# Kernel optimization log

Hardware: AMD Instinct MI355X
Metric: run time of the kernel (lower is better)

Reference implementation:

```python
import jax, jax.numpy as jnp
import numpy as np

N = 50000      # nodes
E = 400000     # edges per relation
R = 3          # edge types
D = 128        # input_dim == hidden_dim
H = 8          # attention heads
Dh = D // H    # per-head dim (16)
OUT = 1        # output logits
NEG_SLOPE = 0.2
LN_EPS = 1e-5


def setup_inputs() -> dict:
    key = jax.random.key(0)
    ks = jax.random.split(key, 20)
    s = 0.05
    f32 = jnp.float32
    return {
        "feat": jax.random.normal(ks[0], (N, D), f32),
        "edge_src": jax.random.randint(ks[1], (R, E), 0, N, dtype=jnp.int32),
        "edge_dst": jax.random.randint(ks[2], (R, E), 0, N, dtype=jnp.int32),
        # conv1: per-relation GATConv params (W, attn_l, attn_r, bias)
        "W1": jax.random.normal(ks[3], (R, D, H * Dh), f32) * s,
        "al1": jax.random.normal(ks[4], (R, H, Dh), f32) * s,
        "ar1": jax.random.normal(ks[5], (R, H, Dh), f32) * s,
        "b1": jnp.zeros((R, H * Dh), f32),
        # conv2
        "W2": jax.random.normal(ks[6], (R, D, H * Dh), f32) * s,
        "al2": jax.random.normal(ks[7], (R, H, Dh), f32) * s,
        "ar2": jax.random.normal(ks[8], (R, H, Dh), f32) * s,
        "b2": jnp.zeros((R, H * Dh), f32),
        # LayerNorm
        "ln_g": jnp.ones((D,), f32),
        "ln_b": jnp.zeros((D,), f32),
        # classifier MLP (dropout inactive at eval)
        "Wc1": jax.random.normal(ks[9], (D, D), f32) * s,
        "bc1": jnp.zeros((D,), f32),
        "Wc2": jax.random.normal(ks[10], (D, OUT), f32) * s,
        "bc2": jnp.zeros((OUT,), f32),
    }


def _gat(x, src, dst, W, al, ar, b):
    """DGL GATConv on one relation: x [N,Din] -> [N, H*Dh]."""
    h = (x @ W).reshape(N, H, Dh)                       # projected feats
    el = (h * al).sum(-1)                               # [N,H] src attn term
    er = (h * ar).sum(-1)                               # [N,H] dst attn term
    e = jax.nn.leaky_relu(el[src] + er[dst], NEG_SLOPE)  # [E,H]
    # edge-softmax over incoming edges per dst node, per head
    m = jax.ops.segment_max(e, dst, num_segments=N)     # [N,H]
    ex = jnp.exp(e - m[dst])
    denom = jax.ops.segment_sum(ex, dst, num_segments=N)
    alpha = ex / denom[dst]                             # [E,H]
    msg = alpha[:, :, None] * h[src]                    # [E,H,Dh]
    out = jax.ops.segment_sum(msg, dst, num_segments=N)  # [N,H,Dh]
    return out.reshape(N, H * Dh) + b


def _hetero(x, edge_src, edge_dst, W, al, ar, b):
    out = jnp.zeros((N, H * Dh), x.dtype)
    for r in range(R):  # small fixed relation count
        out = out + _gat(x, edge_src[r], edge_dst[r], W[r], al[r], ar[r], b[r])
    return out


def reference(feat, edge_src, edge_dst, W1, al1, ar1, b1, W2, al2, ar2, b2,
              ln_g, ln_b, Wc1, bc1, Wc2, bc2):
    h1 = jax.nn.relu(_hetero(feat, edge_src, edge_dst, W1, al1, ar1, b1))
    h2 = _hetero(h1, edge_src, edge_dst, W2, al2, ar2, b2)
    h = h2 + h1
    mu = h.mean(-1, keepdims=True)
    var = ((h - mu) ** 2).mean(-1, keepdims=True)
    h = (h - mu) * jax.lax.rsqrt(var + LN_EPS) * ln_g + ln_b
    h = jax.nn.relu(h @ Wc1 + bc1)
    return h @ Wc2 + bc2
```

## Files before the change

### kernel.cpp

```cpp
#include <hip/hip_runtime.h>
#include <math.h>

#define NN 50000
#define NE 400000
#define NREL 3
#define NCH 196

typedef __bf16 bf16x8 __attribute__((ext_vector_type(8)));
typedef float floatx4 __attribute__((ext_vector_type(4)));

__device__ __forceinline__ unsigned short f2bf(float f) {
  unsigned int u = __float_as_uint(f);
  return (unsigned short)((u + 0x7fffu + ((u >> 16) & 1u)) >> 16);
}

__global__ __launch_bounds__(256) void prep_wt(
    const float* __restrict__ W1, const float* __restrict__ W2,
    const float* __restrict__ Wc1, unsigned short* __restrict__ Wt) {
  int mat = blockIdx.x >> 3, slab = blockIdx.x & 7;
  const float* Wsrc = mat < 3 ? W1 + mat * 16384
                    : (mat < 6 ? W2 + (mat - 3) * 16384 : Wc1);
  unsigned short* dst = Wt + (size_t)mat * 144 * 128;
  int k0 = slab * 16;
#pragma unroll
  for (int i = 0; i < 8; ++i) {
    int idx = i * 256 + threadIdx.x;
    int k = k0 + (idx >> 7), nn = idx & 127;
    dst[nn * 128 + k] = f2bf(Wsrc[k * 128 + nn]);
  }
}

__global__ __launch_bounds__(256) void prep_attn(
    const float* __restrict__ W1, const float* __restrict__ W2,
    const float* __restrict__ al1, const float* __restrict__ ar1,
    const float* __restrict__ al2, const float* __restrict__ ar2,
    unsigned short* __restrict__ Wt) {
  int mat = blockIdx.x;
  const float* Wsrc = mat < 3 ? W1 + mat * 16384 : W2 + (mat - 3) * 16384;
  const float* alp = mat < 3 ? al1 + mat * 128 : al2 + (mat - 3) * 128;
  const float* arp = mat < 3 ? ar1 + mat * 128 : ar2 + (mat - 3) * 128;
  unsigned short* dst = Wt + (size_t)mat * 144 * 128;
#pragma unroll
  for (int i = 0; i < 8; ++i) {
    int j = i * 256 + threadIdx.x;
    int half = j >> 10, jj = j & 1023;
    int k = jj >> 3, h = jj & 7;
    const float* av = half ? arp : alp;
    float s = 0.f;
#pragma unroll
    for (int d = 0; d < 16; ++d) s += Wsrc[k * 128 + h * 16 + d] * av[h * 16 + d];
    dst[(128 + half * 8 + h) * 128 + k] = f2bf(s);
  }
}

__global__ __launch_bounds__(256) void gemm3_attn_mfma(
    const float* __restrict__ X, const unsigned short* __restrict__ Wt,
    unsigned short* __restrict__ hp, float* __restrict__ el,
    float* __restrict__ er, int n) {
  __shared__ unsigned short Xs[64 * 136];
  __shared__ unsigned short Ws[144 * 136];
  int t = threadIdx.x;
  int rowbase = blockIdx.x * 64;

  const float4* X4 = (const float4*)X;
#pragma unroll
  for (int i = 0; i < 8; ++i) {
    int v = t + i * 256;
    int row = v >> 5, k4 = (v & 31) * 4;
    float4 x = make_float4(0.f, 0.f, 0.f, 0.f);
    if (rowbase + row < n) x = X4[(size_t)(rowbase + row) * 32 + (v & 31)];
    ushort4 p;
    p.x = f2bf(x.x); p.y = f2bf(x.y); p.z = f2bf(x.z); p.w = f2bf(x.w);
    *(ushort4*)&Xs[row * 136 + k4] = p;
  }

  int lane = t & 63, wave = t >> 6;
  int quad = lane >> 4, l = lane & 15;

  for (int r = 0; r < NREL; ++r) {
    __syncthreads();
    const uint4* WtR = (const uint4*)(Wt + (size_t)r * 144 * 128);
#pragma unroll
    for (int i = 0; i < 9; ++i) {
      int v = t + i * 256;
      ((uint4*)Ws)[(v >> 4) * 17 + (v & 15)] = WtR[v];
    }
    __syncthreads();

    floatx4 acc[9];
#pragma unroll
    for (int i = 0; i < 9; ++i) acc[i] = floatx4{0.f, 0.f, 0.f, 0.f};
#pragma unroll
    for (int ks = 0; ks < 4; ++ks) {
      bf16x8 a = *(const bf16x8*)&Xs[(wave * 16 + l) * 136 + ks * 32 + quad * 8];
#pragma unroll
      for (int nt = 0; nt < 9; ++nt) {
        bf16x8 b = *(const bf16x8*)&Ws[(nt * 16 + l) * 136 + ks * 32 + quad * 8];
        acc[nt] = __builtin_amdgcn_mfma_f32_16x16x32_bf16(a, b, acc[nt], 0, 0, 0);
      }
    }

    unsigned short* hpR = hp + (size_t)r * NN * 128;
    float* elR = el + (size_t)r * NN * 8;
    float* erR = er + (size_t)r * NN * 8;
    int r0 = rowbase + wave * 16 + quad * 4;
#pragma unroll
    for (int reg = 0; reg < 4; ++reg) {
      int row = r0 + reg;
      if (row < n) {
#pragma unroll
        for (int nt = 0; nt < 8; ++nt)
          hpR[(size_t)row * 128 + nt * 16 + l] = f2bf(acc[nt][reg]);
        if (l < 8) elR[row * 8 + l] = acc[8][reg];
        else       erR[row * 8 + (l - 8)] = acc[8][reg];
      }
    }
  }
}

__global__ __launch_bounds__(256) void gemm_head_mfma(
    const float* __restrict__ X, const unsigned short* __restrict__ Wt,
    const float* __restrict__ bc1, const float* __restrict__ wc2,
    const float* __restrict__ bc2, float* __restrict__ out, int n) {
  __shared__ unsigned short Xs[64 * 136];
  __shared__ unsigned short Ws[128 * 136];
  int t = threadIdx.x;
  int rowbase = blockIdx.x * 64;

  const float4* X4 = (const float4*)X;
#pragma unroll
  for (int i = 0; i < 8; ++i) {
    int v = t + i * 256;
    int row = v >> 5, k4 = (v & 31) * 4;
    float4 x = make_float4(0.f, 0.f, 0.f, 0.f);
    if (rowbase + row < n) x = X4[(size_t)(rowbase + row) * 32 + (v & 31)];
    ushort4 p;
    p.x = f2bf(x.x); p.y = f2bf(x.y); p.z = f2bf(x.z); p.w = f2bf(x.w);
    *(ushort4*)&Xs[row * 136 + k4] = p;
  }
  const uint4* WtR = (const uint4*)Wt;
#pragma unroll
  for (int i = 0; i < 8; ++i) {
    int v = t + i * 256;
    ((uint4*)Ws)[(v >> 4) * 17 + (v & 15)] = WtR[v];
  }
  __syncthreads();

  int lane = t & 63, wave = t >> 6;
  int quad = lane >> 4, l = lane & 15;

  floatx4 acc[8];
#pragma unroll
  for (int i = 0; i < 8; ++i) acc[i] = floatx4{0.f, 0.f, 0.f, 0.f};
#pragma unroll
  for (int ks = 0; ks < 4; ++ks) {
    bf16x8 a = *(const bf16x8*)&Xs[(wave * 16 + l) * 136 + ks * 32 + quad * 8];
#pragma unroll
    for (int nt = 0; nt < 8; ++nt) {
      bf16x8 b = *(const bf16x8*)&Ws[(nt * 16 + l) * 136 + ks * 32 + quad * 8];
      acc[nt] = __builtin_amdgcn_mfma_f32_16x16x32_bf16(a, b, acc[nt], 0, 0, 0);
    }
  }

  float bv[8], wv[8];
#pragma unroll
  for (int nt = 0; nt < 8; ++nt) {
    bv[nt] = bc1[nt * 16 + l];
    wv[nt] = wc2[nt * 16 + l];
  }
  int r0 = rowbase + wave * 16 + quad * 4;
#pragma unroll
  for (int reg = 0; reg < 4; ++reg) {
    float s = 0.f;
#pragma unroll
    for (int nt = 0; nt < 8; ++nt)
      s += fmaxf(acc[nt][reg] + bv[nt], 0.f) * wv[nt];
    s += __shfl_xor(s, 1); s += __shfl_xor(s, 2);
    s += __shfl_xor(s, 4); s += __shfl_xor(s, 8);
    int row = r0 + reg;
    if (l == 0 && row < n) out[row] = s + bc2[0];
  }
}

__global__ __launch_bounds__(256) void hist_kernel(
    const int* __restrict__ edst, int* __restrict__ cnt, int* __restrict__ rank) {
  int t = blockIdx.x * 256 + threadIdx.x;
  if (t >= NREL * NE) return;
  int r = t / NE;
  rank[t] = atomicAdd(&cnt[r * NN + edst[t]], 1);
}

__global__ __launch_bounds__(256) void scan1(
    const int* __restrict__ cnt, int* __restrict__ partials) {
  __shared__ int s[256];
  int r = blockIdx.x / NCH, c = blockIdx.x % NCH;
  int i = c * 256 + threadIdx.x;
  s[threadIdx.x] = (i < NN) ? cnt[r * NN + i] : 0;
  __syncthreads();
  for (int off = 128; off; off >>= 1) {
    if (threadIdx.x < off) s[threadIdx.x] += s[threadIdx.x + off];
    __syncthreads();
  }
  if (threadIdx.x == 0) partials[r * NCH + c] = s[0];
}

__global__ __launch_bounds__(256) void scan2(int* __restrict__ partials) {
  __shared__ int s[256];
  int r = blockIdx.x;
  int t = threadIdx.x;
  int v = (t < NCH) ? partials[r * NCH + t] : 0;
  s[t] = v;
  __syncthreads();
  for (int off = 1; off < 256; off <<= 1) {
    int x = (t >= off) ? s[t - off] : 0;
    __syncthreads();
    s[t] += x;
    __syncthreads();
  }
  if (t < NCH) partials[r * NCH + t] = s[t] - v;
}

__global__ __launch_bounds__(256) void scan3(
    const int* __restrict__ cnt, const int* __restrict__ partials,
    int* __restrict__ rowptr) {
  __shared__ int s[256];
  int r = blockIdx.x / NCH, c = blockIdx.x % NCH;
  int t = threadIdx.x;
  int i = c * 256 + t;
  int v = (i < NN) ? cnt[r * NN + i] : 0;
  s[t] = v;
  __syncthreads();
  for (int off = 1; off < 256; off <<= 1) {
    int x = (t >= off) ? s[t - off] : 0;
    __syncthreads();
    s[t] += x;
    __syncthreads();
  }
  int base = partials[r * NCH + c];
  if (i < NN) rowptr[r * (NN + 1) + i] = base + s[t] - v;
  if (c == NCH - 1 && t == 0) rowptr[r * (NN + 1) + NN] = NE;
}

__global__ __launch_bounds__(256) void scatter_kernel(
    const int* __restrict__ esrc, const int* __restrict__ edst,
    const int* __restrict__ rowptr, const int* __restrict__ rank,
    int* __restrict__ col) {
  int t = blockIdx.x * 256 + threadIdx.x;
  if (t >= NREL * NE) return;
  int r = t / NE;
  int pos = rowptr[r * (NN + 1) + edst[t]] + rank[t];
  col[(size_t)r * NE + pos] = esrc[t];
}

__global__ __launch_bounds__(256) void gather_all(
    const int* __restrict__ rowptr, const int* __restrict__ col,
    const float* __restrict__ el, const float* __restrict__ er,
    const unsigned short* __restrict__ hp, const float* __restrict__ b,
    float* __restrict__ h1, const float* __restrict__ g,
    const float* __restrict__ beta, int mode) {
  int wid = (blockIdx.x * 256 + threadIdx.x) >> 6;
  int lane = threadIdx.x & 63;
  if (wid >= NN) return;
  int h = lane >> 3;
  int eoff = lane & 7;
  int c = lane * 2;
  int lane4 = lane * 4;

  int st0, st1, st2, ee0, ee1, ee2;
  {
    const int* rp = rowptr;
    st0 = rp[wid]; ee0 = rp[wid + 1];
    rp += NN + 1;
    st1 = rp[wid]; ee1 = rp[wid + 1];
    rp += NN + 1;
    st2 = rp[wid]; ee2 = rp[wid + 1];
  }
  float erv0 = er[wid * 8 + h];
  float erv1 = er[(size_t)NN * 8 + wid * 8 + h];
  float erv2 = er[(size_t)2 * NN * 8 + wid * 8 + h];
  float b0x = b[c], b1x = b[128 + c], b2x = b[256 + c];
  float b0y = b[c + 1], b1y = b[128 + c + 1], b2y = b[256 + c + 1];
  float2* hptr = (float2*)&h1[(size_t)wid * 128 + c];
  float2 r1 = make_float2(0.f, 0.f);
  float gx = 0.f, gy = 0.f, btx = 0.f, bty = 0.f;
  if (mode) {
    r1 = *hptr;
    gx = g[c]; gy = g[c + 1];
    btx = beta[c]; bty = beta[c + 1];
  }

  const int* clp0 = col;
  const int* clp1 = col + NE;
  const int* clp2 = col + 2 * NE;
  const float* elp0 = el;
  const float* elp1 = el + (size_t)NN * 8;
  const float* elp2 = el + (size_t)2 * NN * 8;
  const char* hpb0 = (const char*)hp;
  const char* hpb1 = hpb0 + (size_t)NN * 256;
  const char* hpb2 = hpb1 + (size_t)NN * 256;

  int la0 = ee0 - 1; if (la0 < st0) la0 = st0; if (la0 >= NE) la0 = NE - 1;
  int la1 = ee1 - 1; if (la1 < st1) la1 = st1; if (la1 >= NE) la1 = NE - 1;
  int la2 = ee2 - 1; if (la2 < st2) la2 = st2; if (la2 >= NE) la2 = NE - 1;

  int i0 = st0 + eoff, i1 = st1 + eoff, i2 = st2 + eoff;
  int cv0 = clp0[i0 < la0 ? i0 : la0];
  int cv1 = clp1[i1 < la1 ? i1 : la1];
  int cv2 = clp2[i2 < la2 ? i2 : la2];
  float ev0 = elp0[cv0 * 8 + h];
  float ev1 = elp1[cv1 * 8 + h];
  float ev2 = elp2[cv2 * 8 + h];

  int bb0 = st0, bb1 = st1, bb2 = st2;
  float den0 = 0.f, den1 = 0.f, den2 = 0.f;
  float sx0 = 0.f, sy0 = 0.f, sx1 = 0.f, sy1 = 0.f, sx2 = 0.f, sy2 = 0.f;

#define A_PHASE(R)                                                             \
  if (a##R) {                                                                  \
    int ni_ = bb##R + 8 + eoff;                                                \
    cm##R = clp##R[ni_ < la##R ? ni_ : la##R];                                 \
    float e_ = ev##R + erv##R;                                                 \
    e_ = fmaxf(e_, 0.2f * e_);                                                 \
    float x_ = (bb##R + eoff < ee##R) ? __expf(e_) : 0.f;                      \
    den##R += x_;                                                              \
    xi##R = __float_as_uint(x_);                                               \
  }

#define LOAD_EDGE(R, JJ)                                                       \
  {                                                                            \
    int s_ = __builtin_amdgcn_readlane(cv##R, JJ);                             \
    u##R##_##JJ = *(const unsigned int*)(hpb##R + (size_t)s_ * 256 + lane4);   \
  }

#define B_PHASE(R)                                                             \
  if (a##R) {                                                                  \
    LOAD_EDGE(R, 0) LOAD_EDGE(R, 1) LOAD_EDGE(R, 2) LOAD_EDGE(R, 3)            \
    LOAD_EDGE(R, 4) LOAD_EDGE(R, 5) LOAD_EDGE(R, 6) LOAD_EDGE(R, 7)            \
  }

#define FMA_EDGE(R, JJ, PAT)                                                   \
  {                                                                            \
    float xe_ = __uint_as_float(__builtin_amdgcn_ds_swizzle(xi##R, PAT));      \
    sx##R += xe_ * __uint_as_float(u##R##_##JJ << 16);                         \
    sy##R += xe_ * __uint_as_float(u##R##_##JJ & 0xffff0000u);                 \
  }

#define C_PHASE(R)                                                             \
  if (a##R) {                                                                  \
    FMA_EDGE(R, 0, 0x18) FMA_EDGE(R, 1, 0x38) FMA_EDGE(R, 2, 0x58)             \
    FMA_EDGE(R, 3, 0x78) FMA_EDGE(R, 4, 0x98) FMA_EDGE(R, 5, 0xb8)             \
    FMA_EDGE(R, 6, 0xd8) FMA_EDGE(R, 7, 0xf8)                                  \
  }

  for (;;) {
    bool a0 = bb0 < ee0, a1 = bb1 < ee1, a2 = bb2 < ee2;
    if (!(a0 | a1 | a2)) break;
    int cm0 = cv0, cm1 = cv1, cm2 = cv2;
    unsigned int xi0 = 0, xi1 = 0, xi2 = 0;
    unsigned int u0_0, u0_1, u0_2, u0_3, u0_4, u0_5, u0_6, u0_7;
    unsigned int u1_0, u1_1, u1_2, u1_3, u1_4, u1_5, u1_6, u1_7;
    unsigned int u2_0, u2_1, u2_2, u2_3, u2_4, u2_5, u2_6, u2_7;
    A_PHASE(0) A_PHASE(1) A_PHASE(2)
    B_PHASE(0) B_PHASE(1) B_PHASE(2)
    float evn0 = ev0, evn1 = ev1, evn2 = ev2;
    if (a0) evn0 = elp0[cm0 * 8 + h];
    if (a1) evn1 = elp1[cm1 * 8 + h];
    if (a2) evn2 = elp2[cm2 * 8 + h];
    __builtin_amdgcn_sched_barrier(0);
    C_PHASE(0) C_PHASE(1) C_PHASE(2)
    bb0 += 8; bb1 += 8; bb2 += 8;
    cv0 = cm0; cv1 = cm1; cv2 = cm2;
    ev0 = evn0; ev1 = evn1; ev2 = evn2;
  }

#undef A_PHASE
#undef LOAD_EDGE
#undef B_PHASE
#undef FMA_EDGE
#undef C_PHASE

  float ax = 0.f, ay = 0.f;
  if (ee0 > st0) {
    float d = den0;
    d += __shfl_xor(d, 1); d += __shfl_xor(d, 2); d += __shfl_xor(d, 4);
    float inv = 1.f / d;
    ax += sx0 * inv; ay += sy0 * inv;
  }
  if (ee1 > st1) {
    float d = den1;
    d += __shfl_xor(d, 1); d += __shfl_xor(d, 2); d += __shfl_xor(d, 4);
    float inv = 1.f / d;
    ax += sx1 * inv; ay += sy1 * inv;
  }
  if (ee2 > st2) {
    float d = den2;
    d += __shfl_xor(d, 1); d += __shfl_xor(d, 2); d += __shfl_xor(d, 4);
    float inv = 1.f / d;
    ax += sx2 * inv; ay += sy2 * inv;
  }

  float bx = b0x + b1x + b2x;
  float by = b0y + b1y + b2y;
  if (mode == 0) {
    *hptr = make_float2(fmaxf(ax + bx, 0.f), fmaxf(ay + by, 0.f));
  } else {
    float vx = ax + bx + r1.x;
    float vy = ay + by + r1.y;
    float s = vx + vy;
#pragma unroll
    for (int off = 32; off; off >>= 1) s += __shfl_xor(s, off);
    float mu = s * (1.f / 128.f);
    float dx = vx - mu, dy = vy - mu;
    float sq = dx * dx + dy * dy;
#pragma unroll
    for (int off = 32; off; off >>= 1) sq += __shfl_xor(sq, off);
    float rstd = rsqrtf(sq * (1.f / 128.f) + 1e-5f);
    *hptr = make_float2(dx * rstd * gx + btx, dy * rstd * gy + bty);
  }
}

extern "C" void kernel_launch(void* const* d_in, const int* in_sizes, int n_in,
                              void* d_out, int out_size, void* d_ws, size_t ws_size,
                              hipStream_t stream) {
  const float* feat = (const float*)d_in[0];
  const int* esrc = (const int*)d_in[1];
  const int* edst = (const int*)d_in[2];
  const float* W1 = (const float*)d_in[3];
  const float* al1 = (const float*)d_in[4];
  const float* ar1 = (const float*)d_in[5];
  const float* b1 = (const float*)d_in[6];
  const float* W2 = (const float*)d_in[7];
  const float* al2 = (const float*)d_in[8];
  const float* ar2 = (const float*)d_in[9];
  const float* b2 = (const float*)d_in[10];
  const float* lng = (const float*)d_in[11];
  const float* lnb = (const float*)d_in[12];
  const float* Wc1 = (const float*)d_in[13];
  const float* bc1 = (const float*)d_in[14];
  const float* Wc2 = (const float*)d_in[15];
  const float* bc2 = (const float*)d_in[16];
  float* out = (float*)d_out;

  unsigned short* hp = (unsigned short*)d_ws;
  float* el = (float*)(hp + (size_t)3 * NN * 128);
  float* er = el + (size_t)3 * NN * 8;
  float* h1 = er + (size_t)3 * NN * 8;
  int* rowptr = (int*)(h1 + (size_t)NN * 128);
  int* col = rowptr + NREL * (NN + 1);
  int* cnt = col + (size_t)NREL * NE;
  int* partials = cnt + NREL * NN;
  unsigned short* Wt = (unsigned short*)(((uintptr_t)(partials + NREL * NCH) + 15)
                                         & ~(uintptr_t)15);
  int* rank = (int*)el;

  const int gemm_grid = (NN + 63) / 64;
  const int edge_grid = (NREL * NE + 255) / 256;
  const int gg_grid = (NN * 64) / 256;

  prep_wt<<<56, 256, 0, stream>>>(W1, W2, Wc1, Wt);
  prep_attn<<<6, 256, 0, stream>>>(W1, W2, al1, ar1, al2, ar2, Wt);

  (void)hipMemsetAsync(cnt, 0, (size_t)NREL * NN * sizeof(int), stream);
  hist_kernel<<<edge_grid, 256, 0, stream>>>(edst, cnt, rank);
  scan1<<<NREL * NCH, 256, 0, stream>>>(cnt, partials);
  scan2<<<NREL, 256, 0, stream>>>(partials);
  scan3<<<NREL * NCH, 256, 0, stream>>>(cnt, partials, rowptr);
  scatter_kernel<<<edge_grid, 256, 0, stream>>>(esrc, edst, rowptr, rank, col);

  gemm3_attn_mfma<<<gemm_grid, 256, 0, stream>>>(feat, Wt, hp, el, er, NN);
  gather_all<<<gg_grid, 256, 0, stream>>>(rowptr, col, el, er, hp, b1,
                                          h1, nullptr, nullptr, 0);
  gemm3_attn_mfma<<<gemm_grid, 256, 0, stream>>>(
      h1, Wt + (size_t)3 * 144 * 128, hp, el, er, NN);
  gather_all<<<gg_grid, 256, 0, stream>>>(rowptr, col, el, er, hp, b2,
                                          h1, lng, lnb, 1);
  gemm_head_mfma<<<gemm_grid, 256, 0, stream>>>(
      h1, Wt + (size_t)6 * 144 * 128, bc1, Wc2, bc2, out, NN);
}
```

Baseline: 420.2 us.

## Peel first 8-edge chunk of all relations unconditionally, per-relation tail loops

Restructures the gather kernel so the first block of up to 8 edges for all three relations is loaded and accumulated without branching, with all 24 feature loads issued together. The remaining edges are processed in separate per-relation loops. Bias, residual and LayerNorm parameter loads move to the epilogue to free registers during the main gather. The aim is more memory-level parallelism and fewer loop-control branches for the typical low-degree node, at the cost of serialising the relations in the tail and issuing loads for relations that have no edges.

```diff
diff --git a/kernel.cpp b/kernel.cpp
--- a/kernel.cpp
+++ b/kernel.cpp
@@ -266,28 +266,15 @@
   int c = lane * 2;
   int lane4 = lane * 4;
 
-  int st0, st1, st2, ee0, ee1, ee2;
-  {
-    const int* rp = rowptr;
-    st0 = rp[wid]; ee0 = rp[wid + 1];
-    rp += NN + 1;
-    st1 = rp[wid]; ee1 = rp[wid + 1];
-    rp += NN + 1;
-    st2 = rp[wid]; ee2 = rp[wid + 1];
-  }
+  const int* rp0 = rowptr;
+  const int* rp1 = rowptr + (NN + 1);
+  const int* rp2 = rowptr + 2 * (NN + 1);
+  int st0 = rp0[wid], ee0 = rp0[wid + 1];
+  int st1 = rp1[wid], ee1 = rp1[wid + 1];
+  int st2 = rp2[wid], ee2 = rp2[wid + 1];
   float erv0 = er[wid * 8 + h];
   float erv1 = er[(size_t)NN * 8 + wid * 8 + h];
   float erv2 = er[(size_t)2 * NN * 8 + wid * 8 + h];
-  float b0x = b[c], b1x = b[128 + c], b2x = b[256 + c];
-  float b0y = b[c + 1], b1y = b[128 + c + 1], b2y = b[256 + c + 1];
-  float2* hptr = (float2*)&h1[(size_t)wid * 128 + c];
-  float2 r1 = make_float2(0.f, 0.f);
-  float gx = 0.f, gy = 0.f, btx = 0.f, bty = 0.f;
-  if (mode) {
-    r1 = *hptr;
-    gx = g[c]; gy = g[c + 1];
-    btx = beta[c]; bty = beta[c + 1];
-  }
 
   const int* clp0 = col;
   const int* clp1 = col + NE;
@@ -304,80 +291,132 @@
   int la2 = ee2 - 1; if (la2 < st2) la2 = st2; if (la2 >= NE) la2 = NE - 1;
 
   int i0 = st0 + eoff, i1 = st1 + eoff, i2 = st2 + eoff;
+  int j0 = i0 + 8, j1 = i1 + 8, j2 = i2 + 8;
   int cv0 = clp0[i0 < la0 ? i0 : la0];
   int cv1 = clp1[i1 < la1 ? i1 : la1];
   int cv2 = clp2[i2 < la2 ? i2 : la2];
+  int cm0 = clp0[j0 < la0 ? j0 : la0];
+  int cm1 = clp1[j1 < la1 ? j1 : la1];
+  int cm2 = clp2[j2 < la2 ? j2 : la2];
+
   float ev0 = elp0[cv0 * 8 + h];
   float ev1 = elp1[cv1 * 8 + h];
   float ev2 = elp2[cv2 * 8 + h];
 
-  int bb0 = st0, bb1 = st1, bb2 = st2;
-  float den0 = 0.f, den1 = 0.f, den2 = 0.f;
-  float sx0 = 0.f, sy0 = 0.f, sx1 = 0.f, sy1 = 0.f, sx2 = 0.f, sy2 = 0.f;
-
-#define A_PHASE(R)                                                             \
-  if (a##R) {                                                                  \
-    int ni_ = bb##R + 8 + eoff;                                                \
-    cm##R = clp##R[ni_ < la##R ? ni_ : la##R];                                 \
-    float e_ = ev##R + erv##R;                                                 \
-    e_ = fmaxf(e_, 0.2f * e_);                                                 \
-    float x_ = (bb##R + eoff < ee##R) ? __expf(e_) : 0.f;                      \
-    den##R += x_;                                                              \
-    xi##R = __float_as_uint(x_);                                               \
-  }
-
-#define LOAD_EDGE(R, JJ)                                                       \
+  unsigned int u0_0, u0_1, u0_2, u0_3, u0_4, u0_5, u0_6, u0_7;
+  unsigned int u1_0, u1_1, u1_2, u1_3, u1_4, u1_5, u1_6, u1_7;
+  unsigned int u2_0, u2_1, u2_2, u2_3, u2_4, u2_5, u2_6, u2_7;
+
+#define LOAD1(R, JJ)                                                           \
   {                                                                            \
     int s_ = __builtin_amdgcn_readlane(cv##R, JJ);                             \
     u##R##_##JJ = *(const unsigned int*)(hpb##R + (size_t)s_ * 256 + lane4);   \
   }
-
-#define B_PHASE(R)                                                             \
-  if (a##R) {                                                                  \
-    LOAD_EDGE(R, 0) LOAD_EDGE(R, 1) LOAD_EDGE(R, 2) LOAD_EDGE(R, 3)            \
-    LOAD_EDGE(R, 4) LOAD_EDGE(R, 5) LOAD_EDGE(R, 6) LOAD_EDGE(R, 7)            \
-  }
-
-#define FMA_EDGE(R, JJ, PAT)                                                   \
+  LOAD1(0, 0) LOAD1(0, 1) LOAD1(0, 2) LOAD1(0, 3)
+  LOAD1(0, 4) LOAD1(0, 5) LOAD1(0, 6) LOAD1(0, 7)
+  LOAD1(1, 0) LOAD1(1, 1) LOAD1(1, 2) LOAD1(1, 3)
+  LOAD1(1, 4) LOAD1(1, 5) LOAD1(1, 6) LOAD1(1, 7)
+  LOAD1(2, 0) LOAD1(2, 1) LOAD1(2, 2) LOAD1(2, 3)
+  LOAD1(2, 4) LOAD1(2, 5) LOAD1(2, 6) LOAD1(2, 7)
+#undef LOAD1
+
+  float e0 = ev0 + erv0; e0 = fmaxf(e0, 0.2f * e0);
+  float e1 = ev1 + erv1; e1 = fmaxf(e1, 0.2f * e1);
+  float e2 = ev2 + erv2; e2 = fmaxf(e2, 0.2f * e2);
+  float x0 = (i0 < ee0) ? __expf(e0) : 0.f;
+  float x1 = (i1 < ee1) ? __expf(e1) : 0.f;
+  float x2 = (i2 < ee2) ? __expf(e2) : 0.f;
+  float den0 = x0, den1 = x1, den2 = x2;
+  unsigned int xi0 = __float_as_uint(x0);
+  unsigned int xi1 = __float_as_uint(x1);
+  unsigned int xi2 = __float_as_uint(x2);
+
+  float sx0 = 0.f, sy0 = 0.f, sx1 = 0.f, sy1 = 0.f, sx2 = 0.f, sy2 = 0.f;
+
+#define FMA1(R, JJ, PAT)                                                       \
   {                                                                            \
     float xe_ = __uint_as_float(__builtin_amdgcn_ds_swizzle(xi##R, PAT));      \
     sx##R += xe_ * __uint_as_float(u##R##_##JJ << 16);                         \
     sy##R += xe_ * __uint_as_float(u##R##_##JJ & 0xffff0000u);                 \
   }
-
-#define C_PHASE(R)                                                             \
-  if (a##R) {                                                                  \
-    FMA_EDGE(R, 0, 0x18) FMA_EDGE(R, 1, 0x38) FMA_EDGE(R, 2, 0x58)             \
-    FMA_EDGE(R, 3, 0x78) FMA_EDGE(R, 4, 0x98) FMA_EDGE(R, 5, 0xb8)             \
-    FMA_EDGE(R, 6, 0xd8) FMA_EDGE(R, 7, 0xf8)                                  \
-  }
-
-  for (;;) {
-    bool a0 = bb0 < ee0, a1 = bb1 < ee1, a2 = bb2 < ee2;
-    if (!(a0 | a1 | a2)) break;
-    int cm0 = cv0, cm1 = cv1, cm2 = cv2;
-    unsigned int xi0 = 0, xi1 = 0, xi2 = 0;
-    unsigned int u0_0, u0_1, u0_2, u0_3, u0_4, u0_5, u0_6, u0_7;
-    unsigned int u1_0, u1_1, u1_2, u1_3, u1_4, u1_5, u1_6, u1_7;
-    unsigned int u2_0, u2_1, u2_2, u2_3, u2_4, u2_5, u2_6, u2_7;
-    A_PHASE(0) A_PHASE(1) A_PHASE(2)
-    B_PHASE(0) B_PHASE(1) B_PHASE(2)
-    float evn0 = ev0, evn1 = ev1, evn2 = ev2;
-    if (a0) evn0 = elp0[cm0 * 8 + h];
-    if (a1) evn1 = elp1[cm1 * 8 + h];
-    if (a2) evn2 = elp2[cm2 * 8 + h];
-    __builtin_amdgcn_sched_barrier(0);
-    C_PHASE(0) C_PHASE(1) C_PHASE(2)
-    bb0 += 8; bb1 += 8; bb2 += 8;
-    cv0 = cm0; cv1 = cm1; cv2 = cm2;
-    ev0 = evn0; ev1 = evn1; ev2 = evn2;
-  }
-
-#undef A_PHASE
-#undef LOAD_EDGE
-#undef B_PHASE
-#undef FMA_EDGE
-#undef C_PHASE
+  FMA1(0, 0, 0x18) FMA1(0, 1, 0x38) FMA1(0, 2, 0x58) FMA1(0, 3, 0x78)
+  FMA1(0, 4, 0x98) FMA1(0, 5, 0xb8) FMA1(0, 6, 0xd8) FMA1(0, 7, 0xf8)
+  FMA1(1, 0, 0x18) FMA1(1, 1, 0x38) FMA1(1, 2, 0x58) FMA1(1, 3, 0x78)
+  FMA1(1, 4, 0x98) FMA1(1, 5, 0xb8) FMA1(1, 6, 0xd8) FMA1(1, 7, 0xf8)
+  FMA1(2, 0, 0x18) FMA1(2, 1, 0x38) FMA1(2, 2, 0x58) FMA1(2, 3, 0x78)
+  FMA1(2, 4, 0x98) FMA1(2, 5, 0xb8) FMA1(2, 6, 0xd8) FMA1(2, 7, 0xf8)
+#undef FMA1
+
+#define TAIL(R)                                                                \
+  if (st##R + 8 < ee##R) {                                                     \
+    int bb = st##R + 8;                                                        \
+    int cvt = cm##R;                                                           \
+    float evt = elp##R[cvt * 8 + h];                                           \
+    for (;;) {                                                                 \
+      int ni = bb + 8 + eoff;                                                  \
+      int cmt = clp##R[ni < la##R ? ni : la##R];                               \
+      float e_ = evt + erv##R;                                                 \
+      e_ = fmaxf(e_, 0.2f * e_);                                               \
+      float x_ = (bb + eoff < ee##R) ? __expf(e_) : 0.f;                       \
+      den##R += x_;                                                            \
+      unsigned int xt_ = __float_as_uint(x_);                                  \
+      unsigned int t0, t1, t2, t3, t4, t5, t6, t7;                             \
+      {                                                                        \
+        int s_;                                                                \
+        s_ = __builtin_amdgcn_readlane(cvt, 0);                                \
+        t0 = *(const unsigned int*)(hpb##R + (size_t)s_ * 256 + lane4);        \
+        s_ = __builtin_amdgcn_readlane(cvt, 1);                                \
+        t1 = *(const unsigned int*)(hpb##R + (size_t)s_ * 256 + lane4);        \
+        s_ = __builtin_amdgcn_readlane(cvt, 2);                                \
+        t2 = *(const unsigned int*)(hpb##R + (size_t)s_ * 256 + lane4);        \
+        s_ = __builtin_amdgcn_readlane(cvt, 3);                                \
+        t3 = *(const unsigned int*)(hpb##R + (size_t)s_ * 256 + lane4);        \
+        s_ = __builtin_amdgcn_readlane(cvt, 4);                                \
+        t4 = *(const unsigned int*)(hpb##R + (size_t)s_ * 256 + lane4);        \
+        s_ = __builtin_amdgcn_readlane(cvt, 5);                                \
+        t5 = *(const unsigned int*)(hpb##R + (size_t)s_ * 256 + lane4);        \
+        s_ = __builtin_amdgcn_readlane(cvt, 6);                                \
+        t6 = *(const unsigned int*)(hpb##R + (size_t)s_ * 256 + lane4);        \
+        s_ = __builtin_amdgcn_readlane(cvt, 7);                                \
+        t7 = *(const unsigned int*)(hpb##R + (size_t)s_ * 256 + lane4);        \
+      }                                                                        \
+      {                                                                        \
+        float xe_;                                                             \
+        xe_ = __uint_as_float(__builtin_amdgcn_ds_swizzle(xt_, 0x18));         \
+        sx##R += xe_ * __uint_as_float(t0 << 16);                              \
+        sy##R += xe_ * __uint_as_float(t0 & 0xffff0000u);                      \
+        xe_ = __uint_as_float(__builtin_amdgcn_ds_swizzle(xt_, 0x38));         \
+        sx##R += xe_ * __uint_as_float(t1 << 16);                              \
+        sy##R += xe_ * __uint_as_float(t1 & 0xffff0000u);                      \
+        xe_ = __uint_as_float(__builtin_amdgcn_ds_swizzle(xt_, 0x58));         \
+        sx##R += xe_ * __uint_as_float(t2 << 16);                              \
+        sy##R += xe_ * __uint_as_float(t2 & 0xffff0000u);                      \
+        xe_ = __uint_as_float(__builtin_amdgcn_ds_swizzle(xt_, 0x78));         \
+        sx##R += xe_ * __uint_as_float(t3 << 16);                              \
+        sy##R += xe_ * __uint_as_float(t3 & 0xffff0000u);                      \
+        xe_ = __uint_as_float(__builtin_amdgcn_ds_swizzle(xt_, 0x98));         \
+        sx##R += xe_ * __uint_as_float(t4 << 16);                              \
+        sy##R += xe_ * __uint_as_float(t4 & 0xffff0000u);                      \
+        xe_ = __uint_as_float(__builtin_amdgcn_ds_swizzle(xt_, 0xb8));         \
+        sx##R += xe_ * __uint_as_float(t5 << 16);                              \
+        sy##R += xe_ * __uint_as_float(t5 & 0xffff0000u);                      \
+        xe_ = __uint_as_float(__builtin_amdgcn_ds_swizzle(xt_, 0xd8));         \
+        sx##R += xe_ * __uint_as_float(t6 << 16);                              \
+        sy##R += xe_ * __uint_as_float(t6 & 0xffff0000u);                      \
+        xe_ = __uint_as_float(__builtin_amdgcn_ds_swizzle(xt_, 0xf8));         \
+        sx##R += xe_ * __uint_as_float(t7 << 16);                              \
+        sy##R += xe_ * __uint_as_float(t7 & 0xffff0000u);                      \
+      }                                                                        \
+      bb += 8;                                                                 \
+      if (bb >= ee##R) break;                                                  \
+      evt = elp##R[cmt * 8 + h];                                               \
+      cvt = cmt;                                                               \
+    }                                                                          \
+  }
+  TAIL(0)
+  TAIL(1)
+  TAIL(2)
+#undef TAIL
 
   float ax = 0.f, ay = 0.f;
   if (ee0 > st0) {
@@ -399,11 +438,13 @@
     ax += sx2 * inv; ay += sy2 * inv;
   }
 
-  float bx = b0x + b1x + b2x;
-  float by = b0y + b1y + b2y;
+  float bx = b[c] + b[128 + c] + b[256 + c];
+  float by = b[c + 1] + b[128 + c + 1] + b[256 + c + 1];
+  float2* hptr = (float2*)&h1[(size_t)wid * 128 + c];
   if (mode == 0) {
     *hptr = make_float2(fmaxf(ax + bx, 0.f), fmaxf(ay + by, 0.f));
   } else {
+    float2 r1 = *hptr;
     float vx = ax + bx + r1.x;
     float vy = ay + by + r1.y;
     float s = vx + vy;
@@ -415,7 +456,8 @@
 #pragma unroll
     for (int off = 32; off; off >>= 1) sq += __shfl_xor(sq, off);
     float rstd = rsqrtf(sq * (1.f / 128.f) + 1e-5f);
-    *hptr = make_float2(dx * rstd * gx + btx, dy * rstd * gy + bty);
+    *hptr = make_float2(dx * rstd * g[c] + beta[c],
+                        dy * rstd * g[c + 1] + beta[c + 1]);
   }
 }
 
```

Measured after the change: 383.8 us. 1.09x faster.
